# Optimization experiments

Hardware: AMD Instinct MI355X
Metric: run time of the kernel (lower is better)

The kernel has to match this reference:

```python
import jax, jax.numpy as jnp
import numpy as np

NUM_EMBED = 8192
EMBED_DIM = 256


def setup_inputs() -> dict:
    key = jax.random.key(0)
    k1, k2 = jax.random.split(key)
    input_data = jax.random.normal(k1, (32, EMBED_DIM, 32, 32), dtype=jnp.float32)
    codebook = jax.random.normal(k2, (NUM_EMBED, EMBED_DIM), dtype=jnp.float32)
    return {"input_data": input_data, "codebook": codebook}


def reference(input_data, codebook):
    N, C, H, W = input_data.shape
    # NCHW -> NHWC -> [N*H*W, C]
    data = jnp.transpose(input_data, (0, 2, 3, 1)).reshape(-1, C)
    dist = (
        jnp.sum(data * data, axis=1, keepdims=True)          # [T, 1]
        - 2.0 * jnp.einsum("tc,kc->tk", data, codebook)      # [T, K]
        + jnp.sum(codebook * codebook, axis=1)[None, :]       # [1, K]
    )
    embed_ind = jnp.argmin(dist, axis=1)                      # [T]
    quantize = codebook[embed_ind]                            # [T, C] gather
    quantize_detach = data + jax.lax.stop_gradient(quantize - data)
    return quantize, quantize_detach, data
```

## Files before the change

kernel.cpp:

```cpp
#include <hip/hip_runtime.h>
#include <stdint.h>


#define T_TOT 32768
#define K_TOT 8192
#define CD    256
#define SPLITS 4
#define NSPLIT 2048
#define MT    64
#define NTI   32
#define BHALF 16384

typedef _Float16 h8 __attribute__((ext_vector_type(8)));
typedef _Float16 h4 __attribute__((ext_vector_type(4)));
typedef _Float16 h2 __attribute__((ext_vector_type(2)));
typedef float f4 __attribute__((ext_vector_type(4)));
typedef unsigned long long u64;
typedef unsigned int u32;

#define WS_A16   0u
#define WS_B16   16777216u
#define WS_E2    20971520u
#define WS_E2B   21004288u
#define WS_CAND  21037056u
#define WS_NEED  23265280u

__device__ __forceinline__ u64 shfl_xor_u64(u64 v, int off, int w) {
  unsigned lo = (unsigned)v, hi = (unsigned)(v >> 32);
  lo = __shfl_xor(lo, off, w);
  hi = __shfl_xor(hi, off, w);
  return ((u64)hi << 32) | lo;
}
__device__ __forceinline__ u64 umin64(u64 a, u64 b) { return a < b ? a : b; }
__device__ __forceinline__ u64 umax64(u64 a, u64 b) { return a < b ? b : a; }
__device__ __forceinline__ u32 umin32(u32 a, u32 b) { return a < b ? a : b; }
__device__ __forceinline__ u32 umax32(u32 a, u32 b) { return a < b ? b : a; }

__device__ __forceinline__ void gll16(const void* g, void* l) {
  __builtin_amdgcn_global_load_lds(
      (const __attribute__((address_space(1))) void*)g,
      (__attribute__((address_space(3))) void*)l, 16, 0, 0);
}

__device__ __forceinline__ void stage_tile(const _Float16* __restrict__ gsrc,
                                           _Float16* lbase, int w, int lane) {
  const int lrow = lane >> 5, lslot = lane & 31;
  #pragma unroll
  for (int s = 0; s < 8; ++s) {
    const int r0 = s * 8 + w * 2;
    const int r = r0 + lrow;
    const int chunk = lslot ^ (r & 7);
    gll16(gsrc + (u64)r * CD + chunk * 8, lbase + r0 * CD);
  }
}



__global__ __launch_bounds__(256) void cvt_data_kernel(
    const float* __restrict__ in, _Float16* __restrict__ A16) {
  __shared__ float Ds[32][257];
  const int tid = threadIdx.x;
  const int t0 = blockIdx.x * 32;
  const int nbase = (t0 >> 10) << 18;
  const int tin = t0 & 1023;
  #pragma unroll 8
  for (int p = 0; p < 32; ++p) {
    const int lin = p * 256 + tid;
    const int cc = lin >> 5, tt = lin & 31;
    Ds[tt][cc] = in[nbase + cc * 1024 + tin + tt];
  }
  __syncthreads();
  if (tid < 128) {
    for (int tt = 0; tt < 32; ++tt) {
      h2 hv;
      hv[0] = (_Float16)(-Ds[tt][tid * 2]);
      hv[1] = (_Float16)(-Ds[tt][tid * 2 + 1]);
      *(h2*)(A16 + (t0 + tt) * CD + tid * 2) = hv;
    }
  }
}

__global__ __launch_bounds__(256) void cvt_cb_kernel(
    const float* __restrict__ cb, _Float16* __restrict__ B16,
    float* __restrict__ e2, float* __restrict__ e2b) {
  const int tid = threadIdx.x;
  const int w = tid >> 6, lane = tid & 63;
  const int row = blockIdx.x * 4 + w;
  const float4 v = *(const float4*)(cb + row * CD + lane * 4);
  h4 hv; hv[0] = (_Float16)v.x; hv[1] = (_Float16)v.y;
  hv[2] = (_Float16)v.z; hv[3] = (_Float16)v.w;
  *(h4*)(B16 + row * CD + lane * 4) = hv;
  float s = v.x * v.x + v.y * v.y + v.z * v.z + v.w * v.w;
  #pragma unroll
  for (int off = 32; off >= 1; off >>= 1) s += __shfl_xor(s, off, 64);
  if (lane == 0) { e2[row] = s; e2b[row] = 0.5f * s + 256.0f; }
}

__global__ __launch_bounds__(256, 2) void screen_kernel(
    const _Float16* __restrict__ A, const _Float16* __restrict__ B,
    const float* __restrict__ e2b, u64* __restrict__ cand) {
  __shared__ __align__(16) _Float16 smem[2 * BHALF];

  const int tid = threadIdx.x;
  const int lane = tid & 63;
  const int w = tid >> 6;
  const int wrg = w >> 1;
  const int wcg = w & 1;
  const int q = lane >> 4;
  const int c15 = lane & 15;
  const int sx = c15 & 7;

  const int bm = blockIdx.x & 511;
  const int split = blockIdx.x >> 9;
  const int t0 = bm * MT;
  const int n0s = split * NSPLIT;

  _Float16* buf0 = smem;
  _Float16* buf1 = smem + BHALF;

  stage_tile(A + (u64)t0 * CD, buf0, w, lane);
  __syncthreads();

  h8 af[2][8];
  {
    const int m0 = wrg * 32 + c15;
    #pragma unroll
    for (int mi = 0; mi < 2; ++mi) {
      const int m = m0 + mi * 16;
      #pragma unroll
      for (int kk = 0; kk < 8; ++kk) {
        const int slot = (kk * 4 + q) ^ sx;
        af[mi][kk] = *(const h8*)(buf0 + m * CD + slot * 8);
      }
    }
  }
  stage_tile(B + (u64)n0s * CD, buf1, w, lane);

  const float* e2bs = e2b + n0s + wcg * 32 + c15;
  float ev0 = e2bs[0], ev1 = e2bs[16];

  u32 m1[8], m2[8];
  #pragma unroll
  for (int r = 0; r < 8; ++r) { m1[r] = 0xffffffffu; m2[r] = 0xffffffffu; }

  __syncthreads();

  const int nb0 = wcg * 32 + c15;
  for (int nt = 0; nt < NTI; ++nt) {
    _Float16* cur = (nt & 1) ? buf0 : buf1;
    _Float16* nxt = (nt & 1) ? buf1 : buf0;

    if (nt < NTI - 1)
      stage_tile(B + (u64)(n0s + (nt + 1) * 64) * CD, nxt, w, lane);
    const int ntn = (nt < NTI - 1) ? (nt + 1) * 64 : nt * 64;
    const float evn0 = e2bs[ntn];
    const float evn1 = e2bs[ntn + 16];

    f4 acc[2][2];
    #pragma unroll
    for (int mi = 0; mi < 2; ++mi) {
      acc[mi][0] = (f4){ev0, ev0, ev0, ev0};
      acc[mi][1] = (f4){ev1, ev1, ev1, ev1};
    }
    #pragma unroll
    for (int kk = 0; kk < 8; ++kk) {
      const int slot = (kk * 4 + q) ^ sx;
      const h8 b0 = *(const h8*)(cur + nb0 * CD + slot * 8);
      const h8 b1 = *(const h8*)(cur + (nb0 + 16) * CD + slot * 8);
      acc[0][0] = __builtin_amdgcn_mfma_f32_16x16x32_f16(af[0][kk], b0, acc[0][0], 0, 0, 0);
      acc[1][0] = __builtin_amdgcn_mfma_f32_16x16x32_f16(af[1][kk], b0, acc[1][0], 0, 0, 0);
      acc[0][1] = __builtin_amdgcn_mfma_f32_16x16x32_f16(af[0][kk], b1, acc[0][1], 0, 0, 0);
      acc[1][1] = __builtin_amdgcn_mfma_f32_16x16x32_f16(af[1][kk], b1, acc[1][1], 0, 0, 0);
    }

    #pragma unroll
    for (int mi = 0; mi < 2; ++mi)
      #pragma unroll
      for (int reg = 0; reg < 4; ++reg) {
        const int r = mi * 4 + reg;
        const u32 k0 = (__float_as_uint(acc[mi][0][reg]) & ~63u) | (u32)(nt * 2);
        const u32 k1 = (__float_as_uint(acc[mi][1][reg]) & ~63u) | (u32)(nt * 2 + 1);
        const u32 lo = umin32(k0, k1), hi = umax32(k0, k1);
        const u32 t = umax32(m1[r], lo);
        m1[r] = umin32(m1[r], lo);
        m2[r] = umin32(m2[r], umin32(hi, t));
      }
    ev0 = evn0; ev1 = evn1;
    __syncthreads();
  }

  u64 P1[8], P2[8];
  #pragma unroll
  for (int r = 0; r < 8; ++r) {
    const u32 l1 = m1[r] & 63u, l2 = m2[r] & 63u;
    const u32 col1 = (u32)(n0s + (l1 >> 1) * 64 + wcg * 32 + (l1 & 1) * 16 + c15);
    const u32 col2 = (u32)(n0s + (l2 >> 1) * 64 + wcg * 32 + (l2 & 1) * 16 + c15);
    P1[r] = ((u64)m1[r] << 32) | col1;
    P2[r] = ((u64)m2[r] << 32) | col2;
  }
  #pragma unroll
  for (int st = 1; st < 16; st <<= 1) {
    #pragma unroll
    for (int r = 0; r < 8; ++r) {
      const u64 o1 = shfl_xor_u64(P1[r], st, 16);
      const u64 o2 = shfl_xor_u64(P2[r], st, 16);
      const u64 n1 = umin64(P1[r], o1);
      const u64 hi = umax64(P1[r], o1);
      P2[r] = umin64(hi, umin64(P2[r], o2));
      P1[r] = n1;
    }
  }

  u64* mbuf = (u64*)smem;
  if (c15 == 0) {
    #pragma unroll
    for (int r = 0; r < 8; ++r) {
      const int mi = r >> 2, reg = r & 3;
      const int row = wrg * 32 + mi * 16 + q * 4 + reg;
      mbuf[(wcg * 64 + row) * 2 + 0] = P1[r];
      mbuf[(wcg * 64 + row) * 2 + 1] = P2[r];
    }
  }
  __syncthreads();
  if (tid < 64) {
    const u64 a1 = mbuf[tid * 2], a2 = mbuf[tid * 2 + 1];
    const u64 b1 = mbuf[(64 + tid) * 2], b2 = mbuf[(64 + tid) * 2 + 1];
    const u64 n1 = umin64(a1, b1);
    const u64 n2 = umin64(umax64(a1, b1), umin64(a2, b2));
    cand[(u64)(t0 + tid) * 8 + split * 2 + 0] = n1;
    cand[(u64)(t0 + tid) * 8 + split * 2 + 1] = n2;
  }
}

__global__ __launch_bounds__(256) void rescore_output_kernel(
    const float* __restrict__ in, const float* __restrict__ cb,
    const float* __restrict__ e2, const u64* __restrict__ cand,
    float* __restrict__ out) {
  __shared__ __align__(16) float Ds[32][260];
  __shared__ int idxs[32];
  const int tid = threadIdx.x;
  const int t0 = blockIdx.x * 32;
  const int nbase = (t0 >> 10) << 18;
  const int tin = t0 & 1023;
  #pragma unroll 8
  for (int p = 0; p < 32; ++p) {
    const int lin = p * 256 + tid;
    const int cc = lin >> 5, tt = lin & 31;
    Ds[tt][cc] = in[nbase + cc * 1024 + tin + tt];
  }
  __syncthreads();
  const int w = tid >> 6, lane = tid & 63;
  for (int s = 0; s < 8; ++s) {
    const int tt = w * 8 + s;
    const int t = t0 + tt;
    int colv = 0;
    if (lane < 8) colv = (int)(u32)cand[(u64)t * 8 + lane];
    const float4 x = *(const float4*)&Ds[tt][lane * 4];
    float bestd = 1e30f; int bestc = 0x7fffffff;
    #pragma unroll
    for (int j = 0; j < 8; ++j) {
      const int col = __shfl(colv, j, 64);
      const float4 e = *(const float4*)(cb + (u64)col * CD + lane * 4);
      float p4 = x.x * e.x + x.y * e.y + x.z * e.z + x.w * e.w;
      #pragma unroll
      for (int off = 32; off >= 1; off >>= 1) p4 += __shfl_xor(p4, off, 64);
      const float d = e2[col] - 2.0f * p4;
      if (d < bestd || (d == bestd && col < bestc)) { bestd = d; bestc = col; }
    }
    if (lane == 0) idxs[tt] = bestc;
  }
  __syncthreads();
  float* out1 = out;
  float* out2 = out + 8388608;
  float* out3 = out + 16777216;
  for (int tt = 0; tt < 32; ++tt) {
    const float d = Ds[tt][tid];
    const int k = idxs[tt];
    const float qv = cb[k * CD + tid];
    const float qd = d + (qv - d);
    const int o = (t0 + tt) * CD + tid;
    out1[o] = qv;
    out2[o] = qd;
    out3[o] = d;
  }
}


__global__ __launch_bounds__(256) void norms_kernel(const float* __restrict__ in,
                                                    const float* __restrict__ cb,
                                                    float* __restrict__ e2,
                                                    float* __restrict__ x2) {
  const int b = blockIdx.x;
  const int tid = threadIdx.x;
  if (b < 2048) {
    const int wave = tid >> 6, lane = tid & 63;
    const int row = b * 4 + wave;
    const float4 v = *(const float4*)(cb + row * CD + lane * 4);
    float s = v.x * v.x + v.y * v.y + v.z * v.z + v.w * v.w;
    #pragma unroll
    for (int off = 32; off >= 1; off >>= 1) s += __shfl_down(s, off, 64);
    if (lane == 0) e2[row] = s;
  } else {
    const int t = (b - 2048) * 256 + tid;
    const float* p = in + ((t >> 10) << 18) + (t & 1023);
    float s = 0.f;
    #pragma unroll 8
    for (int c = 0; c < CD; ++c) { const float v = p[c << 10]; s += v * v; }
    x2[t] = s;
  }
}

__global__ __launch_bounds__(256) void dist_argmin_kernel(
    const float* __restrict__ in, const float* __restrict__ cb,
    const float* __restrict__ e2, const float* __restrict__ x2,
    u64* __restrict__ packed) {
  __shared__ __align__(16) float As_[32][128];
  __shared__ __align__(16) float Bs_[32][128];
  const int tid = threadIdx.x;
  const int tx = tid & 15, ty = tid >> 4;
  const int tb = blockIdx.x & 255;
  const int ks = blockIdx.x >> 8;
  const int t0 = tb * 128;
  const int nbase = (t0 >> 10) << 18;
  const int tin = t0 & 1023;
  float xi[8];
  #pragma unroll
  for (int i = 0; i < 8; ++i)
    xi[i] = x2[t0 + ty * 4 + (i & 3) + ((i >> 2) << 6)];
  u64 best[8];
  #pragma unroll
  for (int i = 0; i < 8; ++i) best[i] = ~0ull;
  for (int kt = 0; kt < 32; ++kt) {
    const int k0 = ks * 4096 + kt * 128;
    float acc[8][8];
    #pragma unroll
    for (int i = 0; i < 8; ++i)
      #pragma unroll
      for (int j = 0; j < 8; ++j) acc[i][j] = 0.f;
    float ej[8];
    #pragma unroll
    for (int j = 0; j < 8; ++j)
      ej[j] = e2[k0 + tx * 4 + (j & 3) + ((j >> 2) << 6)];
    for (int ch = 0; ch < 8; ++ch) {
      const int c0 = ch * 32;
      #pragma unroll
      for (int p = 0; p < 4; ++p) {
        const int l = p * 1024 + tid * 4;
        const int cc = l >> 7, tt = l & 127;
        *(float4*)&As_[cc][tt] =
            *(const float4*)(in + nbase + (c0 + cc) * 1024 + tin + tt);
      }
      #pragma unroll
      for (int p = 0; p < 4; ++p) {
        const int ix = p * 256 + tid;
        const int kk = ix >> 3, cs = (ix & 7) * 4;
        const float4 v = *(const float4*)(cb + (k0 + kk) * CD + c0 + cs);
        Bs_[cs + 0][kk] = v.x; Bs_[cs + 1][kk] = v.y;
        Bs_[cs + 2][kk] = v.z; Bs_[cs + 3][kk] = v.w;
      }
      __syncthreads();
      #pragma unroll
      for (int cc = 0; cc < 32; ++cc) {
        const float4 a0 = *(const float4*)&As_[cc][ty * 4];
        const float4 a1 = *(const float4*)&As_[cc][64 + ty * 4];
        const float4 b0 = *(const float4*)&Bs_[cc][tx * 4];
        const float4 b1 = *(const float4*)&Bs_[cc][64 + tx * 4];
        const float a[8]  = {a0.x, a0.y, a0.z, a0.w, a1.x, a1.y, a1.z, a1.w};
        const float bb[8] = {b0.x, b0.y, b0.z, b0.w, b1.x, b1.y, b1.z, b1.w};
        #pragma unroll
        for (int i = 0; i < 8; ++i)
          #pragma unroll
          for (int j = 0; j < 8; ++j)
            acc[i][j] += a[i] * bb[j];
      }
      __syncthreads();
    }
    #pragma unroll
    for (int i = 0; i < 8; ++i) {
      u64 m = best[i];
      #pragma unroll
      for (int j = 0; j < 8; ++j) {
        const float dist = (xi[i] - 2.0f * acc[i][j]) + ej[j];
        const int kidx = k0 + tx * 4 + (j & 3) + ((j >> 2) << 6);
        const u64 pk = ((u64)__float_as_uint(dist) << 32) | (unsigned)kidx;
        m = pk < m ? pk : m;
      }
      best[i] = m;
    }
  }
  #pragma unroll
  for (int i = 0; i < 8; ++i) {
    u64 m = best[i];
    #pragma unroll
    for (int off = 8; off >= 1; off >>= 1) {
      const u64 o = shfl_xor_u64(m, off, 16);
      m = o < m ? o : m;
    }
    if (tx == 0)
      atomicMin(&packed[t0 + ty * 4 + (i & 3) + ((i >> 2) << 6)], m);
  }
}

__global__ __launch_bounds__(256) void output_kernel(
    const float* __restrict__ in, const float* __restrict__ cb,
    const u64* __restrict__ packed, float* __restrict__ out) {
  __shared__ float Ds[32][257];
  __shared__ int idxs[32];
  const int tid = threadIdx.x;
  const int t0 = blockIdx.x * 32;
  const int nbase = (t0 >> 10) << 18;
  const int tin = t0 & 1023;
  if (tid < 32) idxs[tid] = (int)(packed[t0 + tid] & 0xffffffffull);
  #pragma unroll 8
  for (int p = 0; p < 32; ++p) {
    const int lin = p * 256 + tid;
    const int cc = lin >> 5, tt = lin & 31;
    Ds[tt][cc] = in[nbase + cc * 1024 + tin + tt];
  }
  __syncthreads();
  float* out1 = out;
  float* out2 = out + 8388608;
  float* out3 = out + 16777216;
  for (int tt = 0; tt < 32; ++tt) {
    const float d = Ds[tt][tid];
    const int k = idxs[tt];
    const float q = cb[k * CD + tid];
    const float qd = d + (q - d);
    const int o = (t0 + tt) * CD + tid;
    out1[o] = q;
    out2[o] = qd;
    out3[o] = d;
  }
}

extern "C" void kernel_launch(void* const* d_in, const int* in_sizes, int n_in,
                              void* d_out, int out_size, void* d_ws, size_t ws_size,
                              hipStream_t stream) {
  const float* in = (const float*)d_in[0];
  const float* cb = (const float*)d_in[1];
  float* out = (float*)d_out;

  if (ws_size >= WS_NEED) {
    _Float16* A16 = (_Float16*)((char*)d_ws + WS_A16);
    _Float16* B16 = (_Float16*)((char*)d_ws + WS_B16);
    float* e2  = (float*)((char*)d_ws + WS_E2);
    float* e2b = (float*)((char*)d_ws + WS_E2B);
    u64* cand  = (u64*)((char*)d_ws + WS_CAND);

    cvt_data_kernel<<<T_TOT / 32, 256, 0, stream>>>(in, A16);
    cvt_cb_kernel<<<K_TOT / 4, 256, 0, stream>>>(cb, B16, e2, e2b);
    screen_kernel<<<(T_TOT / MT) * SPLITS, 256, 0, stream>>>(A16, B16, e2b, cand);
    rescore_output_kernel<<<T_TOT / 32, 256, 0, stream>>>(in, cb, e2, cand, out);
  } else {
    u64* packed = (u64*)d_ws;
    float* e2 = (float*)((char*)d_ws + 262144);
    float* x2 = (float*)((char*)d_ws + 294912);
    hipMemsetAsync(packed, 0xFF, T_TOT * sizeof(u64), stream);
    norms_kernel<<<2176, 256, 0, stream>>>(in, cb, e2, x2);
    dist_argmin_kernel<<<512, 256, 0, stream>>>(in, cb, e2, x2, packed);
    output_kernel<<<T_TOT / 32, 256, 0, stream>>>(in, cb, packed, out);
  }
}
```

Baseline: 337.7 us.

## Prepack fp16 operands into MFMA fragment layout and load directly from global

Result: slower. 404.4 us (+19.7%).

```diff
diff --git a/kernel.cpp b/kernel.cpp
--- a/kernel.cpp
+++ b/kernel.cpp
@@ -9,7 +9,6 @@
 #define NSPLIT 2048
 #define MT    64
 #define NTI   32
-#define BHALF 16384
 
 typedef _Float16 h8 __attribute__((ext_vector_type(8)));
 typedef _Float16 h4 __attribute__((ext_vector_type(4)));
@@ -18,8 +17,8 @@
 typedef unsigned long long u64;
 typedef unsigned int u32;
 
-#define WS_A16   0u
-#define WS_B16   16777216u
+#define WS_AP    0u
+#define WS_BP    16777216u
 #define WS_E2    20971520u
 #define WS_E2B   21004288u
 #define WS_CAND  21037056u
@@ -36,28 +35,10 @@
 __device__ __forceinline__ u32 umin32(u32 a, u32 b) { return a < b ? a : b; }
 __device__ __forceinline__ u32 umax32(u32 a, u32 b) { return a < b ? b : a; }
 
-__device__ __forceinline__ void gll16(const void* g, void* l) {
-  __builtin_amdgcn_global_load_lds(
-      (const __attribute__((address_space(1))) void*)g,
-      (__attribute__((address_space(3))) void*)l, 16, 0, 0);
-}
-
-__device__ __forceinline__ void stage_tile(const _Float16* __restrict__ gsrc,
-                                           _Float16* lbase, int w, int lane) {
-  const int lrow = lane >> 5, lslot = lane & 31;
-  #pragma unroll
-  for (int s = 0; s < 8; ++s) {
-    const int r0 = s * 8 + w * 2;
-    const int r = r0 + lrow;
-    const int chunk = lslot ^ (r & 7);
-    gll16(gsrc + (u64)r * CD + chunk * 8, lbase + r0 * CD);
-  }
-}
-
 
 
 __global__ __launch_bounds__(256) void cvt_data_kernel(
-    const float* __restrict__ in, _Float16* __restrict__ A16) {
+    const float* __restrict__ in, _Float16* __restrict__ Ap) {
   __shared__ float Ds[32][257];
   const int tid = threadIdx.x;
   const int t0 = blockIdx.x * 32;
@@ -70,138 +51,134 @@
     Ds[tt][cc] = in[nbase + cc * 1024 + tin + tt];
   }
   __syncthreads();
-  if (tid < 128) {
-    for (int tt = 0; tt < 32; ++tt) {
-      h2 hv;
-      hv[0] = (_Float16)(-Ds[tt][tid * 2]);
-      hv[1] = (_Float16)(-Ds[tt][tid * 2 + 1]);
-      *(h2*)(A16 + (t0 + tt) * CD + tid * 2) = hv;
-    }
+  const u64 g0 = (u64)(t0 >> 4);
+  #pragma unroll
+  for (int p = 0; p < 4; ++p) {
+    const int id = p * 256 + tid;
+    const int gl = id >> 9, kk = (id >> 6) & 7, l = id & 63;
+    const int row = gl * 16 + (l & 15);
+    const int c0 = kk * 32 + (l >> 4) * 8;
+    h8 hv;
+    #pragma unroll
+    for (int j = 0; j < 8; ++j) hv[j] = (_Float16)(-Ds[row][c0 + j]);
+    *(h8*)(Ap + ((g0 + (u64)gl) * 8 + kk) * 512 + (u64)l * 8) = hv;
   }
 }
 
 __global__ __launch_bounds__(256) void cvt_cb_kernel(
-    const float* __restrict__ cb, _Float16* __restrict__ B16,
+    const float* __restrict__ cb, _Float16* __restrict__ Bp,
     float* __restrict__ e2, float* __restrict__ e2b) {
-  const int tid = threadIdx.x;
+  __shared__ float Cs[16][260];
+  const int tid = threadIdx.x;
+  const int g = blockIdx.x;
+  #pragma unroll
+  for (int r = 0; r < 16; ++r)
+    Cs[r][tid] = cb[((u64)g * 16 + r) * 256 + tid];
+  __syncthreads();
   const int w = tid >> 6, lane = tid & 63;
-  const int row = blockIdx.x * 4 + w;
-  const float4 v = *(const float4*)(cb + row * CD + lane * 4);
-  h4 hv; hv[0] = (_Float16)v.x; hv[1] = (_Float16)v.y;
-  hv[2] = (_Float16)v.z; hv[3] = (_Float16)v.w;
-  *(h4*)(B16 + row * CD + lane * 4) = hv;
-  float s = v.x * v.x + v.y * v.y + v.z * v.z + v.w * v.w;
-  #pragma unroll
-  for (int off = 32; off >= 1; off >>= 1) s += __shfl_xor(s, off, 64);
-  if (lane == 0) { e2[row] = s; e2b[row] = 0.5f * s + 256.0f; }
+  #pragma unroll
+  for (int rr = 0; rr < 4; ++rr) {
+    const int row = w * 4 + rr;
+    const float4 v = *(const float4*)&Cs[row][lane * 4];
+    float s = v.x * v.x + v.y * v.y + v.z * v.z + v.w * v.w;
+    #pragma unroll
+    for (int off = 32; off >= 1; off >>= 1) s += __shfl_xor(s, off, 64);
+    if (lane == 0) {
+      e2[g * 16 + row] = s;
+      e2b[g * 16 + row] = 0.5f * s + 256.0f;
+    }
+  }
+  #pragma unroll
+  for (int p = 0; p < 2; ++p) {
+    const int id = p * 256 + tid;
+    const int kk = id >> 6, l = id & 63;
+    const int row = l & 15, c0 = kk * 32 + (l >> 4) * 8;
+    h8 hv;
+    #pragma unroll
+    for (int j = 0; j < 8; ++j) hv[j] = (_Float16)Cs[row][c0 + j];
+    *(h8*)(Bp + ((u64)g * 8 + kk) * 512 + (u64)l * 8) = hv;
+  }
 }
 
 __global__ __launch_bounds__(256, 2) void screen_kernel(
-    const _Float16* __restrict__ A, const _Float16* __restrict__ B,
+    const _Float16* __restrict__ Ap, const _Float16* __restrict__ Bp,
     const float* __restrict__ e2b, u64* __restrict__ cand) {
-  __shared__ __align__(16) _Float16 smem[2 * BHALF];
+  __shared__ u64 mbuf[4][64][2];
 
   const int tid = threadIdx.x;
   const int lane = tid & 63;
   const int w = tid >> 6;
-  const int wrg = w >> 1;
-  const int wcg = w & 1;
   const int q = lane >> 4;
   const int c15 = lane & 15;
-  const int sx = c15 & 7;
 
   const int bm = blockIdx.x & 511;
   const int split = blockIdx.x >> 9;
   const int t0 = bm * MT;
   const int n0s = split * NSPLIT;
 
-  _Float16* buf0 = smem;
-  _Float16* buf1 = smem + BHALF;
-
-  stage_tile(A + (u64)t0 * CD, buf0, w, lane);
-  __syncthreads();
-
-  h8 af[2][8];
-  {
-    const int m0 = wrg * 32 + c15;
-    #pragma unroll
-    for (int mi = 0; mi < 2; ++mi) {
-      const int m = m0 + mi * 16;
-      #pragma unroll
-      for (int kk = 0; kk < 8; ++kk) {
-        const int slot = (kk * 4 + q) ^ sx;
-        af[mi][kk] = *(const h8*)(buf0 + m * CD + slot * 8);
-      }
-    }
-  }
-  stage_tile(B + (u64)n0s * CD, buf1, w, lane);
-
-  const float* e2bs = e2b + n0s + wcg * 32 + c15;
-  float ev0 = e2bs[0], ev1 = e2bs[16];
-
-  u32 m1[8], m2[8];
-  #pragma unroll
-  for (int r = 0; r < 8; ++r) { m1[r] = 0xffffffffu; m2[r] = 0xffffffffu; }
-
-  __syncthreads();
-
-  const int nb0 = wcg * 32 + c15;
+  const h8* ap = (const h8*)Ap + (u64)(t0 >> 4) * 512 + lane;
+  h8 af[4][8];
+  #pragma unroll
+  for (int mi = 0; mi < 4; ++mi)
+    #pragma unroll
+    for (int kk = 0; kk < 8; ++kk)
+      af[mi][kk] = ap[(mi * 8 + kk) * 64];
+
+  const h8* bp = (const h8*)Bp + ((u64)(n0s >> 4) + (u64)w) * 512 + lane;
+  h8 bf[8];
+  #pragma unroll
+  for (int kk = 0; kk < 8; ++kk) bf[kk] = bp[kk * 64];
+
+  const float* e2p = e2b + n0s + w * 16 + c15;
+  float ev = e2p[0];
+
+  u32 m1[16], m2[16];
+  #pragma unroll
+  for (int r = 0; r < 16; ++r) { m1[r] = 0xffffffffu; m2[r] = 0xffffffffu; }
+
+  #pragma unroll 1
   for (int nt = 0; nt < NTI; ++nt) {
-    _Float16* cur = (nt & 1) ? buf0 : buf1;
-    _Float16* nxt = (nt & 1) ? buf1 : buf0;
-
-    if (nt < NTI - 1)
-      stage_tile(B + (u64)(n0s + (nt + 1) * 64) * CD, nxt, w, lane);
-    const int ntn = (nt < NTI - 1) ? (nt + 1) * 64 : nt * 64;
-    const float evn0 = e2bs[ntn];
-    const float evn1 = e2bs[ntn + 16];
-
-    f4 acc[2][2];
-    #pragma unroll
-    for (int mi = 0; mi < 2; ++mi) {
-      acc[mi][0] = (f4){ev0, ev0, ev0, ev0};
-      acc[mi][1] = (f4){ev1, ev1, ev1, ev1};
-    }
+    const int ntn = (nt < NTI - 1) ? nt + 1 : nt;
+    const float evn = e2p[ntn * 64];
+    const h8* bn = bp + (u64)ntn * 2048;
+    f4 acc[4];
+    #pragma unroll
+    for (int mi = 0; mi < 4; ++mi) acc[mi] = (f4){ev, ev, ev, ev};
     #pragma unroll
     for (int kk = 0; kk < 8; ++kk) {
-      const int slot = (kk * 4 + q) ^ sx;
-      const h8 b0 = *(const h8*)(cur + nb0 * CD + slot * 8);
-      const h8 b1 = *(const h8*)(cur + (nb0 + 16) * CD + slot * 8);
-      acc[0][0] = __builtin_amdgcn_mfma_f32_16x16x32_f16(af[0][kk], b0, acc[0][0], 0, 0, 0);
-      acc[1][0] = __builtin_amdgcn_mfma_f32_16x16x32_f16(af[1][kk], b0, acc[1][0], 0, 0, 0);
-      acc[0][1] = __builtin_amdgcn_mfma_f32_16x16x32_f16(af[0][kk], b1, acc[0][1], 0, 0, 0);
-      acc[1][1] = __builtin_amdgcn_mfma_f32_16x16x32_f16(af[1][kk], b1, acc[1][1], 0, 0, 0);
-    }
-
-    #pragma unroll
-    for (int mi = 0; mi < 2; ++mi)
+      const h8 b = bf[kk];
+      acc[0] = __builtin_amdgcn_mfma_f32_16x16x32_f16(af[0][kk], b, acc[0], 0, 0, 0);
+      acc[1] = __builtin_amdgcn_mfma_f32_16x16x32_f16(af[1][kk], b, acc[1], 0, 0, 0);
+      acc[2] = __builtin_amdgcn_mfma_f32_16x16x32_f16(af[2][kk], b, acc[2], 0, 0, 0);
+      acc[3] = __builtin_amdgcn_mfma_f32_16x16x32_f16(af[3][kk], b, acc[3], 0, 0, 0);
+      bf[kk] = bn[kk * 64];
+    }
+    #pragma unroll
+    for (int mi = 0; mi < 4; ++mi)
       #pragma unroll
       for (int reg = 0; reg < 4; ++reg) {
         const int r = mi * 4 + reg;
-        const u32 k0 = (__float_as_uint(acc[mi][0][reg]) & ~63u) | (u32)(nt * 2);
-        const u32 k1 = (__float_as_uint(acc[mi][1][reg]) & ~63u) | (u32)(nt * 2 + 1);
-        const u32 lo = umin32(k0, k1), hi = umax32(k0, k1);
-        const u32 t = umax32(m1[r], lo);
-        m1[r] = umin32(m1[r], lo);
-        m2[r] = umin32(m2[r], umin32(hi, t));
+        const u32 k = (__float_as_uint(acc[mi][reg]) & ~63u) | (u32)nt;
+        const u32 t = umax32(m1[r], k);
+        m1[r] = umin32(m1[r], k);
+        m2[r] = umin32(m2[r], t);
       }
-    ev0 = evn0; ev1 = evn1;
-    __syncthreads();
-  }
-
-  u64 P1[8], P2[8];
-  #pragma unroll
-  for (int r = 0; r < 8; ++r) {
+    ev = evn;
+  }
+
+  u64 P1[16], P2[16];
+  #pragma unroll
+  for (int r = 0; r < 16; ++r) {
     const u32 l1 = m1[r] & 63u, l2 = m2[r] & 63u;
-    const u32 col1 = (u32)(n0s + (l1 >> 1) * 64 + wcg * 32 + (l1 & 1) * 16 + c15);
-    const u32 col2 = (u32)(n0s + (l2 >> 1) * 64 + wcg * 32 + (l2 & 1) * 16 + c15);
+    const u32 col1 = (u32)(n0s + (int)l1 * 64 + w * 16 + c15);
+    const u32 col2 = (u32)(n0s + (int)l2 * 64 + w * 16 + c15);
     P1[r] = ((u64)m1[r] << 32) | col1;
     P2[r] = ((u64)m2[r] << 32) | col2;
   }
   #pragma unroll
   for (int st = 1; st < 16; st <<= 1) {
     #pragma unroll
-    for (int r = 0; r < 8; ++r) {
+    for (int r = 0; r < 16; ++r) {
       const u64 o1 = shfl_xor_u64(P1[r], st, 16);
       const u64 o2 = shfl_xor_u64(P2[r], st, 16);
       const u64 n1 = umin64(P1[r], o1);
@@ -210,23 +187,27 @@
       P1[r] = n1;
     }
   }
-
-  u64* mbuf = (u64*)smem;
   if (c15 == 0) {
     #pragma unroll
-    for (int r = 0; r < 8; ++r) {
+    for (int r = 0; r < 16; ++r) {
       const int mi = r >> 2, reg = r & 3;
-      const int row = wrg * 32 + mi * 16 + q * 4 + reg;
-      mbuf[(wcg * 64 + row) * 2 + 0] = P1[r];
-      mbuf[(wcg * 64 + row) * 2 + 1] = P2[r];
+      const int row = mi * 16 + q * 4 + reg;
+      mbuf[w][row][0] = P1[r];
+      mbuf[w][row][1] = P2[r];
     }
   }
   __syncthreads();
   if (tid < 64) {
-    const u64 a1 = mbuf[tid * 2], a2 = mbuf[tid * 2 + 1];
-    const u64 b1 = mbuf[(64 + tid) * 2], b2 = mbuf[(64 + tid) * 2 + 1];
-    const u64 n1 = umin64(a1, b1);
-    const u64 n2 = umin64(umax64(a1, b1), umin64(a2, b2));
+    const u64 a1 = mbuf[0][tid][0], a2 = mbuf[0][tid][1];
+    const u64 b1 = mbuf[1][tid][0], b2 = mbuf[1][tid][1];
+    const u64 c1 = mbuf[2][tid][0], c2 = mbuf[2][tid][1];
+    const u64 d1 = mbuf[3][tid][0], d2 = mbuf[3][tid][1];
+    const u64 x1 = umin64(a1, b1);
+    const u64 x2 = umin64(umax64(a1, b1), umin64(a2, b2));
+    const u64 y1 = umin64(c1, d1);
+    const u64 y2 = umin64(umax64(c1, d1), umin64(c2, d2));
+    const u64 n1 = umin64(x1, y1);
+    const u64 n2 = umin64(umax64(x1, y1), umin64(x2, y2));
     cand[(u64)(t0 + tid) * 8 + split * 2 + 0] = n1;
     cand[(u64)(t0 + tid) * 8 + split * 2 + 1] = n2;
   }
@@ -441,15 +422,15 @@
   float* out = (float*)d_out;
 
   if (ws_size >= WS_NEED) {
-    _Float16* A16 = (_Float16*)((char*)d_ws + WS_A16);
-    _Float16* B16 = (_Float16*)((char*)d_ws + WS_B16);
+    _Float16* Ap = (_Float16*)((char*)d_ws + WS_AP);
+    _Float16* Bp = (_Float16*)((char*)d_ws + WS_BP);
     float* e2  = (float*)((char*)d_ws + WS_E2);
     float* e2b = (float*)((char*)d_ws + WS_E2B);
     u64* cand  = (u64*)((char*)d_ws + WS_CAND);
 
-    cvt_data_kernel<<<T_TOT / 32, 256, 0, stream>>>(in, A16);
-    cvt_cb_kernel<<<K_TOT / 4, 256, 0, stream>>>(cb, B16, e2, e2b);
-    screen_kernel<<<(T_TOT / MT) * SPLITS, 256, 0, stream>>>(A16, B16, e2b, cand);
+    cvt_data_kernel<<<T_TOT / 32, 256, 0, stream>>>(in, Ap);
+    cvt_cb_kernel<<<K_TOT / 16, 256, 0, stream>>>(cb, Bp, e2, e2b);
+    screen_kernel<<<(T_TOT / MT) * SPLITS, 256, 0, stream>>>(Ap, Bp, e2b, cand);
     rescore_output_kernel<<<T_TOT / 32, 256, 0, stream>>>(in, cb, e2, cand, out);
   } else {
     u64* packed = (u64*)d_ws;
```
